# Kernel tuning notes

Hardware: AMD Instinct MI355X
Metric: run time of the kernel (lower is better)

## Reference

```python
import jax, jax.numpy as jnp
import numpy as np

B, S, D = 2, 2048, 2048
H = 16
Q_LORA, KV_LORA = 1536, 512
D_NOPE, D_ROPE = 128, 64
D_QK = D_NOPE + D_ROPE  # 192
D_V = 128
EPS = 1e-6
SCALE = D_QK ** -0.5


def rms_norm(x, w):
    var = jnp.mean(jnp.square(x), axis=-1, keepdims=True)
    return x * jax.lax.rsqrt(var + EPS) * w


def apply_rotary_emb(x, freqs_cis):
    # x: [B, S, h, dr]; freqs_cis: [S, dr//2, 2] (cos, sin); interleaved pairs
    b, s, h, dr = x.shape
    xp = x.reshape(b, s, h, dr // 2, 2)
    x0, x1 = xp[..., 0], xp[..., 1]
    cos = freqs_cis[None, :, None, :, 0]
    sin = freqs_cis[None, :, None, :, 1]
    o0 = x0 * cos - x1 * sin
    o1 = x0 * sin + x1 * cos
    return jnp.stack([o0, o1], axis=-1).reshape(b, s, h, dr)


def setup_inputs() -> dict:
    key = jax.random.key(0)
    ks = jax.random.split(key, 8)
    std = 0.02
    x = jax.random.normal(ks[0], (B, S, D), jnp.float32)
    inv_freq = 1.0 / (10000.0 ** (np.arange(0, D_ROPE, 2, dtype=np.float32) / D_ROPE))
    ang = np.outer(np.arange(S, dtype=np.float32), inv_freq)  # [S, 32]
    freqs_cis = jnp.asarray(np.stack([np.cos(ang), np.sin(ang)], axis=-1))
    return {
        'x': x,
        'freqs_cis': freqs_cis,
        'Wqa': jax.random.normal(ks[1], (Q_LORA, D), jnp.float32) * std,
        'q_a_ln_w': jnp.ones((Q_LORA,), jnp.float32),
        'Wqb': jax.random.normal(ks[2], (H * D_QK, Q_LORA), jnp.float32) * std,
        'Wkva': jax.random.normal(ks[3], (KV_LORA + D_ROPE, D), jnp.float32) * std,
        'kv_a_ln_w': jnp.ones((KV_LORA,), jnp.float32),
        'Wkvb': jax.random.normal(ks[4], (H * (D_NOPE + D_V), KV_LORA), jnp.float32) * std,
        'Wo': jax.random.normal(ks[5], (D, H * D_V), jnp.float32) * std,
    }


def reference(x, freqs_cis, Wqa, q_a_ln_w, Wqb, Wkva, kv_a_ln_w, Wkvb, Wo):
    # Low-rank Q projection: down -> RMSNorm -> up
    q = rms_norm(jnp.einsum('bsd,rd->bsr', x, Wqa), q_a_ln_w)
    q = jnp.einsum('bsr,er->bse', q, Wqb).reshape(B, S, H, D_QK)
    q_nope, q_pe = q[..., :D_NOPE], q[..., D_NOPE:]
    q = jnp.concatenate([q_nope, apply_rotary_emb(q_pe, freqs_cis)], axis=-1)

    # Low-rank KV projection with shared (MQA) rope part
    kv = jnp.einsum('bsd,ed->bse', x, Wkva)
    kv_c, k_pe = kv[..., :KV_LORA], kv[..., KV_LORA:]
    kv_c = rms_norm(kv_c, kv_a_ln_w)
    k_pe = apply_rotary_emb(k_pe[:, :, None, :], freqs_cis)  # [B,S,1,D_ROPE]
    kv = jnp.einsum('bsr,er->bse', kv_c, Wkvb).reshape(B, S, H, D_NOPE + D_V)
    k_nope, v = kv[..., :D_NOPE], kv[..., D_NOPE:]
    k = jnp.concatenate(
        [k_nope, jnp.broadcast_to(k_pe, (B, S, H, D_ROPE))], axis=-1)

    # Causal SDPA with scale = qk_head_dim ** -0.5
    scores = jnp.einsum('bqhd,bkhd->bhqk', q, k) * SCALE
    causal = jnp.tril(jnp.ones((S, S), bool))
    scores = jnp.where(causal[None, None], scores, jnp.finfo(scores.dtype).min)
    probs = jax.nn.softmax(scores, axis=-1)
    out = jnp.einsum('bhqk,bkhd->bqhd', probs, v).reshape(B, S, H * D_V)
    return jnp.einsum('bse,de->bsd', out, Wo)
```

## Files before the change

### kernel.cpp

```cpp
#include <hip/hip_runtime.h>
#include <math.h>

#define B_ 2
#define S_ 2048
#define D_ 2048
#define H_ 16
#define QLORA 1536
#define KVLORA 512
#define DN 128
#define DR 64
#define DQK 192
#define DV 128
#define EPSF 1e-6f
#define SCALEF 0.07216878364870322f

typedef short short8 __attribute__((ext_vector_type(8)));
typedef float float4v __attribute__((ext_vector_type(4)));

__device__ __forceinline__ unsigned short f2bf(float f) {
    union { float f; unsigned u; } x; x.f = f;
    unsigned r = x.u + 0x7fffu + ((x.u >> 16) & 1u);
    return (unsigned short)(r >> 16);
}
__device__ __forceinline__ float bf2f(unsigned short u) {
    union { unsigned u; float f; } x; x.u = (unsigned)u << 16;
    return x.f;
}

#define GLD16(src, dst)                                                        \
    __builtin_amdgcn_global_load_lds(                                          \
        (const __attribute__((address_space(1))) void*)(src),                  \
        (__attribute__((address_space(3))) void*)(dst), 16, 0, 0)

__global__ __launch_bounds__(256) void conv_all(
        const float* __restrict__ s0, unsigned short* __restrict__ d0, long e0,
        const float* __restrict__ s1, unsigned short* __restrict__ d1, long e1,
        const float* __restrict__ s2, unsigned short* __restrict__ d2, long e2,
        const float* __restrict__ s3, unsigned short* __restrict__ d3, long e3,
        const float* __restrict__ s4, unsigned short* __restrict__ d4, long e4,
        const float* __restrict__ s5, unsigned short* __restrict__ d5) {
    long c = (long)blockIdx.x * 256 + threadIdx.x;
    const float* src;
    unsigned short* dst;
    if      (c < e0) { src = s0; dst = d0; }
    else if (c < e1) { src = s1; dst = d1; c -= e0; }
    else if (c < e2) { src = s2; dst = d2; c -= e1; }
    else if (c < e3) { src = s3; dst = d3; c -= e2; }
    else if (c < e4) { src = s4; dst = d4; c -= e3; }
    else             { src = s5; dst = d5; c -= e4; }
    const float* p = src + c * 8;
    float4 a = *(const float4*)(p);
    float4 b = *(const float4*)(p + 4);
    union { short8 v; unsigned short u[8]; } t;
    t.u[0] = f2bf(a.x); t.u[1] = f2bf(a.y); t.u[2] = f2bf(a.z); t.u[3] = f2bf(a.w);
    t.u[4] = f2bf(b.x); t.u[5] = f2bf(b.y); t.u[6] = f2bf(b.z); t.u[7] = f2bf(b.w);
    *(short8*)&dst[c * 8] = t.v;
}

#define GBM 128
#define GBN 128
#define GBK 64

template <typename OT>
__global__ __launch_bounds__(256) void gemm_t(const unsigned short* __restrict__ A,
                                              const unsigned short* __restrict__ W,
                                              OT* __restrict__ C,
                                              int M, int N, int K) {
    __shared__ unsigned short As[GBM * GBK];
    __shared__ unsigned short Ws[GBN * GBK];

    const int tid = threadIdx.x;
    const int w = tid >> 6, lane = tid & 63;
    const int l16 = lane & 15, quad = lane >> 4;
    const int wm = (w >> 1) * 64, wn = (w & 1) * 64;
    const int row0 = blockIdx.y * GBM, col0 = blockIdx.x * GBN;

    const int rL  = lane >> 3;
    const int c8g = (lane & 7) ^ rL;
    const int swzk[2] = { (((0 * 4) + quad) ^ (l16 & 7)) * 8,
                          (((1 * 4) + quad) ^ (l16 & 7)) * 8 };

    const float4v zf = {0.f, 0.f, 0.f, 0.f};
    float4v acc[4][4] = {{zf, zf, zf, zf}, {zf, zf, zf, zf},
                         {zf, zf, zf, zf}, {zf, zf, zf, zf}};

    for (int k0 = 0; k0 < K; k0 += GBK) {
        __syncthreads();
#pragma unroll
        for (int j = 0; j < 4; ++j) {
            const int ch = w * 4 + j;
            const int r = ch * 8 + rL;
            GLD16(&A[(size_t)(row0 + r) * K + k0 + c8g * 8], &As[ch * 512]);
            GLD16(&W[(size_t)(col0 + r) * K + k0 + c8g * 8], &Ws[ch * 512]);
        }
        __syncthreads();

#pragma unroll
        for (int kk = 0; kk < 2; ++kk) {
            const int swz = swzk[kk];
            short8 af[4], bf[4];
#pragma unroll
            for (int mi = 0; mi < 4; ++mi)
                af[mi] = *(const short8*)&As[(wm + mi * 16 + l16) * GBK + swz];
#pragma unroll
            for (int ni = 0; ni < 4; ++ni)
                bf[ni] = *(const short8*)&Ws[(wn + ni * 16 + l16) * GBK + swz];
#pragma unroll
            for (int mi = 0; mi < 4; ++mi)
#pragma unroll
                for (int ni = 0; ni < 4; ++ni)
                    acc[mi][ni] = __builtin_amdgcn_mfma_f32_16x16x32_bf16(af[mi], bf[ni], acc[mi][ni], 0, 0, 0);
        }
    }

#pragma unroll
    for (int mi = 0; mi < 4; ++mi)
#pragma unroll
        for (int ni = 0; ni < 4; ++ni)
#pragma unroll
            for (int r = 0; r < 4; ++r) {
                size_t idx = (size_t)(row0 + wm + mi * 16 + quad * 4 + r) * N + col0 + wn + ni * 16 + l16;
                if constexpr (sizeof(OT) == 2) C[idx] = f2bf(acc[mi][ni][r]);
                else                           C[idx] = acc[mi][ni][r];
            }
}

__global__ __launch_bounds__(256) void rmsnorm_b(const float* __restrict__ X,
                                                 const float* __restrict__ w,
                                                 unsigned short* __restrict__ Y,
                                                 int n, int ld) {
    __shared__ float tmp[4];
    const int row = blockIdx.x;
    const int tid = threadIdx.x;
    const float* x = X + (size_t)row * ld;

    float ss = 0.f;
    for (int c = tid; c < n; c += 256) {
        float v = x[c];
        ss = fmaf(v, v, ss);
    }
#pragma unroll
    for (int off = 32; off; off >>= 1) ss += __shfl_xor(ss, off, 64);
    if ((tid & 63) == 0) tmp[tid >> 6] = ss;
    __syncthreads();
    ss = tmp[0] + tmp[1] + tmp[2] + tmp[3];
    float r = rsqrtf(ss / (float)n + EPSF);

    for (int c = tid; c < n; c += 256)
        Y[(size_t)row * n + c] = f2bf(x[c] * r * w[c]);
}

__global__ __launch_bounds__(256) void kv_post(const float* __restrict__ KV,
                                               const float* __restrict__ w,
                                               const float* __restrict__ fc,
                                               unsigned short* __restrict__ kvcb,
                                               float* __restrict__ kpe,
                                               int ldkv) {
    __shared__ float tmp[4];
    const int row = blockIdx.x;
    const int s = row & (S_ - 1);
    const int tid = threadIdx.x;
    const float* kv = KV + (size_t)row * ldkv;

    float ss = 0.f;
#pragma unroll
    for (int c = tid; c < KVLORA; c += 256) {
        float v = kv[c];
        ss = fmaf(v, v, ss);
    }
#pragma unroll
    for (int off = 32; off; off >>= 1) ss += __shfl_xor(ss, off, 64);
    if ((tid & 63) == 0) tmp[tid >> 6] = ss;
    __syncthreads();
    ss = tmp[0] + tmp[1] + tmp[2] + tmp[3];
    float r = rsqrtf(ss / (float)KVLORA + EPSF);

#pragma unroll
    for (int c = tid; c < KVLORA; c += 256)
        kvcb[(size_t)row * KVLORA + c] = f2bf(kv[c] * r * w[c]);

    if (tid < 32) {
        int i = tid;
        float c0 = fc[(s * 32 + i) * 2 + 0];
        float s0 = fc[(s * 32 + i) * 2 + 1];
        float x0 = kv[KVLORA + 2 * i];
        float x1 = kv[KVLORA + 2 * i + 1];
        kpe[(size_t)row * DR + 2 * i]     = x0 * c0 - x1 * s0;
        kpe[(size_t)row * DR + 2 * i + 1] = x0 * s0 + x1 * c0;
    }
}

__global__ __launch_bounds__(256) void pack_k(const unsigned short* __restrict__ kvbb,
                                              const float* __restrict__ kpe,
                                              unsigned short* __restrict__ Kbf) {
    const int c = blockIdx.x * 256 + threadIdx.x;
    const int total = B_ * H_ * S_ * (DQK / 8);
    if (c >= total) return;
    const int d8 = c % (DQK / 8);
    const int hs = c / (DQK / 8);
    const int s  = hs % S_;
    const int bh = hs / S_;
    const int b  = bh / H_;
    const int h  = bh % H_;
    const int d  = d8 * 8;
    const int row = b * S_ + s;

    short8 v;
    if (d < DN) {
        v = *(const short8*)&kvbb[(size_t)row * (H_ * 256) + h * 256 + d];
    } else {
        const float* src = kpe + (size_t)row * DR + (d - DN);
        float4 a = *(const float4*)(src);
        float4 bb = *(const float4*)(src + 4);
        union { short8 v; unsigned short u[8]; } t;
        t.u[0] = f2bf(a.x);  t.u[1] = f2bf(a.y);  t.u[2] = f2bf(a.z);  t.u[3] = f2bf(a.w);
        t.u[4] = f2bf(bb.x); t.u[5] = f2bf(bb.y); t.u[6] = f2bf(bb.z); t.u[7] = f2bf(bb.w);
        v = t.v;
    }
    *(short8*)&Kbf[(size_t)c * 8] = v;
}

__global__ __launch_bounds__(256) void pack_vt(const unsigned short* __restrict__ kvbb,
                                               unsigned short* __restrict__ Vt) {
    __shared__ unsigned short T[DV][72];
    const int st = blockIdx.x;
    const int bh = blockIdx.y;
    const int b = bh >> 4, h = bh & 15;
    const int s0 = st * 64;
    const int tid = threadIdx.x;

    for (int c = tid; c < 64 * 16; c += 256) {
        int sp = c >> 4, ch = c & 15;
        short8 v = *(const short8*)&kvbb[(size_t)(b * S_ + s0 + sp) * (H_ * 256) + h * 256 + DN + ch * 8];
        union { short8 v; unsigned short u[8]; } t; t.v = v;
        int dv = ch * 8;
#pragma unroll
        for (int e = 0; e < 8; ++e) T[dv + e][sp] = t.u[e];
    }
    __syncthreads();
    for (int c = tid; c < 128 * 8; c += 256) {
        int dv = c >> 3, ch = c & 7;
        *(short8*)&Vt[((size_t)bh * DV + dv) * S_ + s0 + ch * 8] = *(short8*)&T[dv][ch * 8];
    }
}

#define KROW 200
#define VROW 72
#define PROW 72
#define NQT 32

__global__ __launch_bounds__(256, 2) void flash_mfma(const unsigned short* __restrict__ Qb,
                                                     const float* __restrict__ fc,
                                                     const unsigned short* __restrict__ Kbf,
                                                     const unsigned short* __restrict__ Vt,
                                                     unsigned short* __restrict__ Ob) {
    __shared__ unsigned short Ks[64][KROW];
    __shared__ unsigned short Vs[DV][VROW];
    __shared__ unsigned short Ps[4][16][PROW];

    const int bh = blockIdx.x;
    const int bx = blockIdx.y;
    const int b = bh >> 4, h = bh & 15;
    const int tid = threadIdx.x;
    const int w = tid >> 6, lane = tid & 63;
    const int l16 = lane & 15, quad = lane >> 4;

    const unsigned short* Kg = Kbf + (size_t)bh * S_ * DQK;
    const unsigned short* Vg = Vt + (size_t)bh * DV * S_;

    for (int half = 0; half < 2; ++half) {
        const int qt = half ? (NQT - 1 - bx) : bx;
        const int q0 = qt * 64;
        const int ntiles = qt + 1;
        const int s = q0 + w * 16 + l16;

        short8 a_q[6];
        {
            const unsigned short* qrow = Qb + (size_t)(b * S_ + s) * (H_ * DQK) + h * DQK;
#pragma unroll
            for (int i = 0; i < 6; ++i) {
                short8 t = *(const short8*)&qrow[i * 32 + quad * 8];
                if (i >= 4) {
                    union { short8 v; unsigned short u[8]; } x; x.v = t;
#pragma unroll
                    for (int j = 0; j < 4; ++j) {
                        int ip = (i - 4) * 16 + quad * 4 + j;
                        float c0 = fc[(s * 32 + ip) * 2 + 0];
                        float s0 = fc[(s * 32 + ip) * 2 + 1];
                        float x0 = bf2f(x.u[2 * j]);
                        float x1 = bf2f(x.u[2 * j + 1]);
                        x.u[2 * j]     = f2bf(x0 * c0 - x1 * s0);
                        x.u[2 * j + 1] = f2bf(x0 * s0 + x1 * c0);
                    }
                    t = x.v;
                }
                a_q[i] = t;
            }
        }

        const float4v zf = {0.f, 0.f, 0.f, 0.f};
        float4v o_acc[8] = {zf, zf, zf, zf, zf, zf, zf, zf};
        float l_r[4] = {0.f, 0.f, 0.f, 0.f};

        short8 ldK[6], ldV[4];
#pragma unroll
        for (int i = 0; i < 6; ++i) {
            int c = tid + i * 256;
            int r = c / 24, cc = c % 24;
            ldK[i] = *(const short8*)&Kg[(size_t)r * DQK + cc * 8];
        }
#pragma unroll
        for (int i = 0; i < 4; ++i) {
            int c = tid + i * 256;
            int r = c >> 3, cc = c & 7;
            ldV[i] = *(const short8*)&Vg[(size_t)r * S_ + cc * 8];
        }

        for (int kt = 0; kt < ntiles; ++kt) {
            const int kbase = kt * 64;
            __syncthreads();
#pragma unroll
            for (int i = 0; i < 6; ++i) {
                int c = tid + i * 256;
                int r = c / 24, cc = c % 24;
                *(short8*)&Ks[r][cc * 8] = ldK[i];
            }
#pragma unroll
            for (int i = 0; i < 4; ++i) {
                int c = tid + i * 256;
                int r = c >> 3, cc = c & 7;
                *(short8*)&Vs[r][cc * 8] = ldV[i];
            }
            if (kt + 1 < ntiles) {
                const int kb2 = kbase + 64;
#pragma unroll
                for (int i = 0; i < 6; ++i) {
                    int c = tid + i * 256;
                    int r = c / 24, cc = c % 24;
                    ldK[i] = *(const short8*)&Kg[(size_t)(kb2 + r) * DQK + cc * 8];
                }
#pragma unroll
                for (int i = 0; i < 4; ++i) {
                    int c = tid + i * 256;
                    int r = c >> 3, cc = c & 7;
                    ldV[i] = *(const short8*)&Vg[(size_t)r * S_ + kb2 + cc * 8];
                }
            }
            __syncthreads();

            float4v sc[4] = {zf, zf, zf, zf};
#pragma unroll
            for (int kg = 0; kg < 4; ++kg) {
#pragma unroll
                for (int i = 0; i < 6; ++i) {
                    short8 bk = *(const short8*)&Ks[kg * 16 + l16][i * 32 + quad * 8];
                    sc[kg] = __builtin_amdgcn_mfma_f32_16x16x32_bf16(a_q[i], bk, sc[kg], 0, 0, 0);
                }
            }

            const bool last = (kt == ntiles - 1);
#pragma unroll
            for (int kg = 0; kg < 4; ++kg) {
                int key = kbase + kg * 16 + l16;
#pragma unroll
                for (int r = 0; r < 4; ++r) {
                    float sv = sc[kg][r] * SCALEF;
                    if (last && key > q0 + w * 16 + quad * 4 + r) sv = -1e30f;
                    float p = __expf(sv);
                    l_r[r] += p;
                    Ps[w][quad * 4 + r][kg * 16 + l16] = f2bf(p);
                }
            }

            __syncthreads();

#pragma unroll
            for (int kc = 0; kc < 2; ++kc) {
                short8 pa = *(const short8*)&Ps[w][l16][kc * 32 + quad * 8];
#pragma unroll
                for (int dvt = 0; dvt < 8; ++dvt) {
                    short8 vb = *(const short8*)&Vs[dvt * 16 + l16][kc * 32 + quad * 8];
                    o_acc[dvt] = __builtin_amdgcn_mfma_f32_16x16x32_bf16(pa, vb, o_acc[dvt], 0, 0, 0);
                }
            }
        }

#pragma unroll
        for (int r = 0; r < 4; ++r) {
            float t = l_r[r];
            t += __shfl_xor(t, 1);
            t += __shfl_xor(t, 2);
            t += __shfl_xor(t, 4);
            t += __shfl_xor(t, 8);
            l_r[r] = t;
        }
#pragma unroll
        for (int r = 0; r < 4; ++r) {
            float inv = 1.f / l_r[r];
            int row = q0 + w * 16 + quad * 4 + r;
            unsigned short* op = Ob + (size_t)(b * S_ + row) * (H_ * DV) + h * DV;
#pragma unroll
            for (int dvt = 0; dvt < 8; ++dvt)
                op[dvt * 16 + l16] = f2bf(o_acc[dvt][r] * inv);
        }
    }
}

extern "C" void kernel_launch(void* const* d_in, const int* in_sizes, int n_in,
                              void* d_out, int out_size, void* d_ws, size_t ws_size,
                              hipStream_t stream) {
    const float* x    = (const float*)d_in[0];
    const float* fc   = (const float*)d_in[1];
    const float* Wqa  = (const float*)d_in[2];
    const float* qlw  = (const float*)d_in[3];
    const float* Wqb  = (const float*)d_in[4];
    const float* Wkva = (const float*)d_in[5];
    const float* kvw  = (const float*)d_in[6];
    const float* Wkvb = (const float*)d_in[7];
    const float* Wo   = (const float*)d_in[8];
    float* out = (float*)d_out;

    const int M = B_ * S_;
    const int NQKV = QLORA + 640;
    char* wsb = (char*)d_ws;

    unsigned short* qb  = (unsigned short*)wsb;
    unsigned short* Wob = (unsigned short*)(wsb + 25165824);
    char* R2 = wsb + 50331648;
    float*          qlkv  = (float*)R2;
    unsigned short* xb    = (unsigned short*)(R2 + 35651584);
    unsigned short* Wcat  = (unsigned short*)(R2 + 52428800);
    unsigned short* kvbb  = (unsigned short*)R2;
    unsigned short* attnb = (unsigned short*)R2;
    char* R3 = R2 + 67108864;
    unsigned short* qlatb = (unsigned short*)R3;
    unsigned short* Wqbb  = (unsigned short*)(R3 + 12582912);
    unsigned short* Kbf   = (unsigned short*)R3;
    char* R4 = R3 + 25165824;
    float*          kpe   = (float*)R4;
    unsigned short* kvcb  = (unsigned short*)(R4 + 1048576);
    unsigned short* Wkvbb = (unsigned short*)(R4 + 5242880);
    unsigned short* Vt    = (unsigned short*)R4;

    {
        const long e0 = 1048576;
        const long e1 = e0 + 393216;
        const long e2 = e1 + 147456;
        const long e3 = e2 + 589824;
        const long e4 = e3 + 262144;
        const long tot = e4 + 524288;
        conv_all<<<(int)(tot / 256), 256, 0, stream>>>(
            x, xb, e0,
            Wqa, Wcat, e1,
            Wkva, Wcat + (size_t)QLORA * D_, e2,
            Wqb, Wqbb, e3,
            Wkvb, Wkvbb, e4,
            Wo, Wob);
    }

    gemm_t<float><<<dim3(NQKV / GBN, M / GBM), 256, 0, stream>>>(xb, Wcat, qlkv, M, NQKV, D_);

    rmsnorm_b<<<M, 256, 0, stream>>>(qlkv, qlw, qlatb, QLORA, NQKV);
    kv_post<<<M, 256, 0, stream>>>(qlkv + QLORA, kvw, fc, kvcb, kpe, NQKV);

    gemm_t<unsigned short><<<dim3(H_ * DQK / GBN, M / GBM), 256, 0, stream>>>(qlatb, Wqbb, qb, M, H_ * DQK, QLORA);
    gemm_t<unsigned short><<<dim3(H_ * 256 / GBN, M / GBM), 256, 0, stream>>>(kvcb, Wkvbb, kvbb, M, H_ * 256, KVLORA);

    {
        int total = B_ * H_ * S_ * (DQK / 8);
        pack_k<<<(total + 255) / 256, 256, 0, stream>>>(kvbb, kpe, Kbf);
        pack_vt<<<dim3(S_ / 64, B_ * H_), 256, 0, stream>>>(kvbb, Vt);
    }

    flash_mfma<<<dim3(B_ * H_, NQT / 2), 256, 0, stream>>>(qb, fc, Kbf, Vt, attnb);

    gemm_t<float><<<dim3(D_ / GBN, M / GBM), 256, 0, stream>>>(attnb, Wob, out, M, D_, D_);
}
```

Measured before the change: 449.8 us.

## Split long causal query tiles across KV halves and merge K/V pack kernels

Causal flash attention now launches one block per short query tile and two blocks per long query tile. Each of the two blocks covers half of the KV range and writes unnormalized fp32 partial outputs and row sums. A new combine kernel sums the two halves and normalizes them. Separately, the K pack and V transpose kernels are fused into one launch. The goal is finer, more even work per block and one fewer launch, at the cost of fp32 partial-output traffic, an extra combine kernel, and a reshuffled workspace layout.

Measured after the change: 488.7 us. 8.6% more time.

```diff
diff --git a/kernel.cpp b/kernel.cpp
--- a/kernel.cpp
+++ b/kernel.cpp
@@ -190,57 +190,58 @@
     }
 }
 
-__global__ __launch_bounds__(256) void pack_k(const unsigned short* __restrict__ kvbb,
-                                              const float* __restrict__ kpe,
-                                              unsigned short* __restrict__ Kbf) {
-    const int c = blockIdx.x * 256 + threadIdx.x;
-    const int total = B_ * H_ * S_ * (DQK / 8);
-    if (c >= total) return;
-    const int d8 = c % (DQK / 8);
-    const int hs = c / (DQK / 8);
-    const int s  = hs % S_;
-    const int bh = hs / S_;
-    const int b  = bh / H_;
-    const int h  = bh % H_;
-    const int d  = d8 * 8;
-    const int row = b * S_ + s;
-
-    short8 v;
-    if (d < DN) {
-        v = *(const short8*)&kvbb[(size_t)row * (H_ * 256) + h * 256 + d];
-    } else {
-        const float* src = kpe + (size_t)row * DR + (d - DN);
-        float4 a = *(const float4*)(src);
-        float4 bb = *(const float4*)(src + 4);
-        union { short8 v; unsigned short u[8]; } t;
-        t.u[0] = f2bf(a.x);  t.u[1] = f2bf(a.y);  t.u[2] = f2bf(a.z);  t.u[3] = f2bf(a.w);
-        t.u[4] = f2bf(bb.x); t.u[5] = f2bf(bb.y); t.u[6] = f2bf(bb.z); t.u[7] = f2bf(bb.w);
-        v = t.v;
-    }
-    *(short8*)&Kbf[(size_t)c * 8] = v;
-}
-
-__global__ __launch_bounds__(256) void pack_vt(const unsigned short* __restrict__ kvbb,
+#define NPK (B_ * H_ * S_ * (DQK / 8) / 256)
+
+__global__ __launch_bounds__(256) void pack_kv(const unsigned short* __restrict__ kvbb,
+                                               const float* __restrict__ kpe,
+                                               unsigned short* __restrict__ Kbf,
                                                unsigned short* __restrict__ Vt) {
     __shared__ unsigned short T[DV][72];
-    const int st = blockIdx.x;
-    const int bh = blockIdx.y;
-    const int b = bh >> 4, h = bh & 15;
-    const int s0 = st * 64;
     const int tid = threadIdx.x;
-
-    for (int c = tid; c < 64 * 16; c += 256) {
-        int sp = c >> 4, ch = c & 15;
-        short8 v = *(const short8*)&kvbb[(size_t)(b * S_ + s0 + sp) * (H_ * 256) + h * 256 + DN + ch * 8];
-        union { short8 v; unsigned short u[8]; } t; t.v = v;
-        int dv = ch * 8;
-#pragma unroll
-        for (int e = 0; e < 8; ++e) T[dv + e][sp] = t.u[e];
-    }
-    __syncthreads();
-    for (int c = tid; c < 128 * 8; c += 256) {
-        int dv = c >> 3, ch = c & 7;
-        *(short8*)&Vt[((size_t)bh * DV + dv) * S_ + s0 + ch * 8] = *(short8*)&T[dv][ch * 8];
+    if ((int)blockIdx.x < NPK) {
+        const int c = blockIdx.x * 256 + tid;
+        const int d8 = c % (DQK / 8);
+        const int hs = c / (DQK / 8);
+        const int s  = hs % S_;
+        const int bh = hs / S_;
+        const int b  = bh / H_;
+        const int h  = bh % H_;
+        const int d  = d8 * 8;
+        const int row = b * S_ + s;
+
+        short8 v;
+        if (d < DN) {
+            v = *(const short8*)&kvbb[(size_t)row * (H_ * 256) + h * 256 + d];
+        } else {
+            const float* src = kpe + (size_t)row * DR + (d - DN);
+            float4 a = *(const float4*)(src);
+            float4 bb = *(const float4*)(src + 4);
+            union { short8 v; unsigned short u[8]; } t;
+            t.u[0] = f2bf(a.x);  t.u[1] = f2bf(a.y);  t.u[2] = f2bf(a.z);  t.u[3] = f2bf(a.w);
+            t.u[4] = f2bf(bb.x); t.u[5] = f2bf(bb.y); t.u[6] = f2bf(bb.z); t.u[7] = f2bf(bb.w);
+            v = t.v;
+        }
+        *(short8*)&Kbf[(size_t)c * 8] = v;
+    } else {
+        const int id = blockIdx.x - NPK;
+        const int st = id & 31;
+        const int bh = id >> 5;
+        const int b = bh >> 4, h = bh & 15;
+        const int s0 = st * 64;
+
+        for (int c = tid; c < 64 * 16; c += 256) {
+            int sp = c >> 4, ch = c & 15;
+            short8 v = *(const short8*)&kvbb[(size_t)(b * S_ + s0 + sp) * (H_ * 256) + h * 256 + DN + ch * 8];
+            union { short8 v; unsigned short u[8]; } t; t.v = v;
+            int dv = ch * 8;
+#pragma unroll
+            for (int e = 0; e < 8; ++e) T[dv + e][sp] = t.u[e];
+        }
+        __syncthreads();
+        for (int c = tid; c < 128 * 8; c += 256) {
+            int dv = c >> 3, ch = c & 7;
+            *(short8*)&Vt[((size_t)bh * DV + dv) * S_ + s0 + ch * 8] = *(short8*)&T[dv][ch * 8];
+        }
     }
 }
 
@@ -249,151 +250,165 @@
 #define PROW 72
 #define NQT 32
 
-__global__ __launch_bounds__(256, 2) void flash_mfma(const unsigned short* __restrict__ Qb,
-                                                     const float* __restrict__ fc,
-                                                     const unsigned short* __restrict__ Kbf,
-                                                     const unsigned short* __restrict__ Vt,
-                                                     unsigned short* __restrict__ Ob) {
+__global__ __launch_bounds__(256, 2) void flash_split(const unsigned short* __restrict__ Qb,
+                                                      const float* __restrict__ fc,
+                                                      const unsigned short* __restrict__ Kbf,
+                                                      const unsigned short* __restrict__ Vt,
+                                                      unsigned short* __restrict__ Ob,
+                                                      float* __restrict__ Opart,
+                                                      float* __restrict__ Lpart) {
     __shared__ unsigned short Ks[64][KROW];
     __shared__ unsigned short Vs[DV][VROW];
     __shared__ unsigned short Ps[4][16][PROW];
 
     const int bh = blockIdx.x;
-    const int bx = blockIdx.y;
+    const int u  = blockIdx.y;
     const int b = bh >> 4, h = bh & 15;
     const int tid = threadIdx.x;
     const int w = tid >> 6, lane = tid & 63;
     const int l16 = lane & 15, quad = lane >> 4;
 
+    int qt, kt0, kt1, slot;
+    bool partial;
+    if (u < 16) { qt = u; kt0 = 0; kt1 = u + 1; partial = false; slot = 0; }
+    else {
+        int idx = u - 16;
+        qt = 16 + (idx >> 1);
+        slot = idx & 1;
+        int nt = qt + 1, mid = nt >> 1;
+        kt0 = slot ? mid : 0;
+        kt1 = slot ? nt : mid;
+        partial = true;
+    }
+    const int q0 = qt * 64;
+
     const unsigned short* Kg = Kbf + (size_t)bh * S_ * DQK;
     const unsigned short* Vg = Vt + (size_t)bh * DV * S_;
 
-    for (int half = 0; half < 2; ++half) {
-        const int qt = half ? (NQT - 1 - bx) : bx;
-        const int q0 = qt * 64;
-        const int ntiles = qt + 1;
-        const int s = q0 + w * 16 + l16;
-
-        short8 a_q[6];
-        {
-            const unsigned short* qrow = Qb + (size_t)(b * S_ + s) * (H_ * DQK) + h * DQK;
-#pragma unroll
-            for (int i = 0; i < 6; ++i) {
-                short8 t = *(const short8*)&qrow[i * 32 + quad * 8];
-                if (i >= 4) {
-                    union { short8 v; unsigned short u[8]; } x; x.v = t;
-#pragma unroll
-                    for (int j = 0; j < 4; ++j) {
-                        int ip = (i - 4) * 16 + quad * 4 + j;
-                        float c0 = fc[(s * 32 + ip) * 2 + 0];
-                        float s0 = fc[(s * 32 + ip) * 2 + 1];
-                        float x0 = bf2f(x.u[2 * j]);
-                        float x1 = bf2f(x.u[2 * j + 1]);
-                        x.u[2 * j]     = f2bf(x0 * c0 - x1 * s0);
-                        x.u[2 * j + 1] = f2bf(x0 * s0 + x1 * c0);
-                    }
-                    t = x.v;
+    const int s = q0 + w * 16 + l16;
+
+    short8 a_q[6];
+    {
+        const unsigned short* qrow = Qb + (size_t)(b * S_ + s) * (H_ * DQK) + h * DQK;
+#pragma unroll
+        for (int i = 0; i < 6; ++i) {
+            short8 t = *(const short8*)&qrow[i * 32 + quad * 8];
+            if (i >= 4) {
+                union { short8 v; unsigned short u[8]; } x; x.v = t;
+#pragma unroll
+                for (int j = 0; j < 4; ++j) {
+                    int ip = (i - 4) * 16 + quad * 4 + j;
+                    float c0 = fc[(s * 32 + ip) * 2 + 0];
+                    float s0 = fc[(s * 32 + ip) * 2 + 1];
+                    float x0 = bf2f(x.u[2 * j]);
+                    float x1 = bf2f(x.u[2 * j + 1]);
+                    x.u[2 * j]     = f2bf(x0 * c0 - x1 * s0);
+                    x.u[2 * j + 1] = f2bf(x0 * s0 + x1 * c0);
                 }
-                a_q[i] = t;
-            }
-        }
-
-        const float4v zf = {0.f, 0.f, 0.f, 0.f};
-        float4v o_acc[8] = {zf, zf, zf, zf, zf, zf, zf, zf};
-        float l_r[4] = {0.f, 0.f, 0.f, 0.f};
-
-        short8 ldK[6], ldV[4];
+                t = x.v;
+            }
+            a_q[i] = t;
+        }
+    }
+
+    const float4v zf = {0.f, 0.f, 0.f, 0.f};
+    float4v o_acc[8] = {zf, zf, zf, zf, zf, zf, zf, zf};
+    float l_r[4] = {0.f, 0.f, 0.f, 0.f};
+
+    short8 ldK[6], ldV[4];
+#pragma unroll
+    for (int i = 0; i < 6; ++i) {
+        int c = tid + i * 256;
+        int r = c / 24, cc = c % 24;
+        ldK[i] = *(const short8*)&Kg[(size_t)(kt0 * 64 + r) * DQK + cc * 8];
+    }
+#pragma unroll
+    for (int i = 0; i < 4; ++i) {
+        int c = tid + i * 256;
+        int r = c >> 3, cc = c & 7;
+        ldV[i] = *(const short8*)&Vg[(size_t)r * S_ + kt0 * 64 + cc * 8];
+    }
+
+    for (int kt = kt0; kt < kt1; ++kt) {
+        const int kbase = kt * 64;
+        __syncthreads();
 #pragma unroll
         for (int i = 0; i < 6; ++i) {
             int c = tid + i * 256;
             int r = c / 24, cc = c % 24;
-            ldK[i] = *(const short8*)&Kg[(size_t)r * DQK + cc * 8];
+            *(short8*)&Ks[r][cc * 8] = ldK[i];
         }
 #pragma unroll
         for (int i = 0; i < 4; ++i) {
             int c = tid + i * 256;
             int r = c >> 3, cc = c & 7;
-            ldV[i] = *(const short8*)&Vg[(size_t)r * S_ + cc * 8];
-        }
-
-        for (int kt = 0; kt < ntiles; ++kt) {
-            const int kbase = kt * 64;
-            __syncthreads();
+            *(short8*)&Vs[r][cc * 8] = ldV[i];
+        }
+        if (kt + 1 < kt1) {
+            const int kb2 = kbase + 64;
 #pragma unroll
             for (int i = 0; i < 6; ++i) {
                 int c = tid + i * 256;
                 int r = c / 24, cc = c % 24;
-                *(short8*)&Ks[r][cc * 8] = ldK[i];
+                ldK[i] = *(const short8*)&Kg[(size_t)(kb2 + r) * DQK + cc * 8];
             }
 #pragma unroll
             for (int i = 0; i < 4; ++i) {
                 int c = tid + i * 256;
                 int r = c >> 3, cc = c & 7;
-                *(short8*)&Vs[r][cc * 8] = ldV[i];
-            }
-            if (kt + 1 < ntiles) {
-                const int kb2 = kbase + 64;
-#pragma unroll
-                for (int i = 0; i < 6; ++i) {
-                    int c = tid + i * 256;
-                    int r = c / 24, cc = c % 24;
-                    ldK[i] = *(const short8*)&Kg[(size_t)(kb2 + r) * DQK + cc * 8];
-                }
-#pragma unroll
-                for (int i = 0; i < 4; ++i) {
-                    int c = tid + i * 256;
-                    int r = c >> 3, cc = c & 7;
-                    ldV[i] = *(const short8*)&Vg[(size_t)r * S_ + kb2 + cc * 8];
-                }
-            }
-            __syncthreads();
-
-            float4v sc[4] = {zf, zf, zf, zf};
-#pragma unroll
-            for (int kg = 0; kg < 4; ++kg) {
-#pragma unroll
-                for (int i = 0; i < 6; ++i) {
-                    short8 bk = *(const short8*)&Ks[kg * 16 + l16][i * 32 + quad * 8];
-                    sc[kg] = __builtin_amdgcn_mfma_f32_16x16x32_bf16(a_q[i], bk, sc[kg], 0, 0, 0);
-                }
-            }
-
-            const bool last = (kt == ntiles - 1);
-#pragma unroll
-            for (int kg = 0; kg < 4; ++kg) {
-                int key = kbase + kg * 16 + l16;
-#pragma unroll
-                for (int r = 0; r < 4; ++r) {
-                    float sv = sc[kg][r] * SCALEF;
-                    if (last && key > q0 + w * 16 + quad * 4 + r) sv = -1e30f;
-                    float p = __expf(sv);
-                    l_r[r] += p;
-                    Ps[w][quad * 4 + r][kg * 16 + l16] = f2bf(p);
-                }
-            }
-
-            __syncthreads();
-
-#pragma unroll
-            for (int kc = 0; kc < 2; ++kc) {
-                short8 pa = *(const short8*)&Ps[w][l16][kc * 32 + quad * 8];
-#pragma unroll
-                for (int dvt = 0; dvt < 8; ++dvt) {
-                    short8 vb = *(const short8*)&Vs[dvt * 16 + l16][kc * 32 + quad * 8];
-                    o_acc[dvt] = __builtin_amdgcn_mfma_f32_16x16x32_bf16(pa, vb, o_acc[dvt], 0, 0, 0);
-                }
-            }
-        }
-
-#pragma unroll
-        for (int r = 0; r < 4; ++r) {
-            float t = l_r[r];
-            t += __shfl_xor(t, 1);
-            t += __shfl_xor(t, 2);
-            t += __shfl_xor(t, 4);
-            t += __shfl_xor(t, 8);
-            l_r[r] = t;
-        }
+                ldV[i] = *(const short8*)&Vg[(size_t)r * S_ + kb2 + cc * 8];
+            }
+        }
+        __syncthreads();
+
+        float4v sc[4] = {zf, zf, zf, zf};
+#pragma unroll
+        for (int kg = 0; kg < 4; ++kg) {
+#pragma unroll
+            for (int i = 0; i < 6; ++i) {
+                short8 bk = *(const short8*)&Ks[kg * 16 + l16][i * 32 + quad * 8];
+                sc[kg] = __builtin_amdgcn_mfma_f32_16x16x32_bf16(a_q[i], bk, sc[kg], 0, 0, 0);
+            }
+        }
+
+        const bool diag = (kt == qt);
+#pragma unroll
+        for (int kg = 0; kg < 4; ++kg) {
+            int key = kbase + kg * 16 + l16;
+#pragma unroll
+            for (int r = 0; r < 4; ++r) {
+                float sv = sc[kg][r] * SCALEF;
+                if (diag && key > q0 + w * 16 + quad * 4 + r) sv = -1e30f;
+                float p = __expf(sv);
+                l_r[r] += p;
+                Ps[w][quad * 4 + r][kg * 16 + l16] = f2bf(p);
+            }
+        }
+
+        __syncthreads();
+
+#pragma unroll
+        for (int kc = 0; kc < 2; ++kc) {
+            short8 pa = *(const short8*)&Ps[w][l16][kc * 32 + quad * 8];
+#pragma unroll
+            for (int dvt = 0; dvt < 8; ++dvt) {
+                short8 vb = *(const short8*)&Vs[dvt * 16 + l16][kc * 32 + quad * 8];
+                o_acc[dvt] = __builtin_amdgcn_mfma_f32_16x16x32_bf16(pa, vb, o_acc[dvt], 0, 0, 0);
+            }
+        }
+    }
+
+#pragma unroll
+    for (int r = 0; r < 4; ++r) {
+        float t = l_r[r];
+        t += __shfl_xor(t, 1);
+        t += __shfl_xor(t, 2);
+        t += __shfl_xor(t, 4);
+        t += __shfl_xor(t, 8);
+        l_r[r] = t;
+    }
+
+    if (!partial) {
 #pragma unroll
         for (int r = 0; r < 4; ++r) {
             float inv = 1.f / l_r[r];
@@ -403,6 +418,39 @@
             for (int dvt = 0; dvt < 8; ++dvt)
                 op[dvt * 16 + l16] = f2bf(o_acc[dvt][r] * inv);
         }
+    } else {
+        const size_t sb = ((size_t)(bh * 16 + (qt - 16)) * 2 + slot);
+        float* ob = Opart + sb * 8192;
+#pragma unroll
+        for (int r = 0; r < 4; ++r) {
+            int row = w * 16 + quad * 4 + r;
+#pragma unroll
+            for (int dvt = 0; dvt < 8; ++dvt)
+                ob[(size_t)row * DV + dvt * 16 + l16] = o_acc[dvt][r];
+            if (l16 == 0) Lpart[sb * 64 + row] = l_r[r];
+        }
+    }
+}
+
+__global__ __launch_bounds__(256) void norm_comb(const float* __restrict__ Opart,
+                                                 const float* __restrict__ Lpart,
+                                                 unsigned short* __restrict__ Ob) {
+    __shared__ float ls[64];
+    const int t = blockIdx.x;
+    const int bh = t >> 4, j = t & 15;
+    const int qt = 16 + j;
+    const int b = bh >> 4, h = bh & 15;
+    const int tid = threadIdx.x;
+    const size_t ob0 = (size_t)t * 2 * 8192, ob1 = ob0 + 8192;
+    const size_t lb0 = (size_t)t * 2 * 64, lb1 = lb0 + 64;
+
+    if (tid < 64) ls[tid] = Lpart[lb0 + tid] + Lpart[lb1 + tid];
+    __syncthreads();
+
+    for (int idx = tid; idx < 64 * DV; idx += 256) {
+        int row = idx >> 7, col = idx & 127;
+        float o = Opart[ob0 + idx] + Opart[ob1 + idx];
+        Ob[(size_t)(b * S_ + qt * 64 + row) * (H_ * DV) + h * DV + col] = f2bf(o / ls[row]);
     }
 }
 
@@ -426,20 +474,22 @@
 
     unsigned short* qb  = (unsigned short*)wsb;
     unsigned short* Wob = (unsigned short*)(wsb + 25165824);
+    float*          kpe = (float*)(wsb + 33554432);
     char* R2 = wsb + 50331648;
     float*          qlkv  = (float*)R2;
     unsigned short* xb    = (unsigned short*)(R2 + 35651584);
     unsigned short* Wcat  = (unsigned short*)(R2 + 52428800);
     unsigned short* kvbb  = (unsigned short*)R2;
     unsigned short* attnb = (unsigned short*)R2;
+    float*          Opart = (float*)(R2 + 16777216);
+    float*          Lpart = (float*)(R2 + 50331648);
     char* R3 = R2 + 67108864;
     unsigned short* qlatb = (unsigned short*)R3;
     unsigned short* Wqbb  = (unsigned short*)(R3 + 12582912);
     unsigned short* Kbf   = (unsigned short*)R3;
     char* R4 = R3 + 25165824;
-    float*          kpe   = (float*)R4;
-    unsigned short* kvcb  = (unsigned short*)(R4 + 1048576);
-    unsigned short* Wkvbb = (unsigned short*)(R4 + 5242880);
+    unsigned short* kvcb  = (unsigned short*)R4;
+    unsigned short* Wkvbb = (unsigned short*)(R4 + 4194304);
     unsigned short* Vt    = (unsigned short*)R4;
 
     {
@@ -466,13 +516,11 @@
     gemm_t<unsigned short><<<dim3(H_ * DQK / GBN, M / GBM), 256, 0, stream>>>(qlatb, Wqbb, qb, M, H_ * DQK, QLORA);
     gemm_t<unsigned short><<<dim3(H_ * 256 / GBN, M / GBM), 256, 0, stream>>>(kvcb, Wkvbb, kvbb, M, H_ * 256, KVLORA);
 
-    {
-        int total = B_ * H_ * S_ * (DQK / 8);
-        pack_k<<<(total + 255) / 256, 256, 0, stream>>>(kvbb, kpe, Kbf);
-        pack_vt<<<dim3(S_ / 64, B_ * H_), 256, 0, stream>>>(kvbb, Vt);
-    }
-
-    flash_mfma<<<dim3(B_ * H_, NQT / 2), 256, 0, stream>>>(qb, fc, Kbf, Vt, attnb);
+    pack_kv<<<NPK + 1024, 256, 0, stream>>>(kvbb, kpe, Kbf, Vt);
+
+    flash_split<<<dim3(B_ * H_, 48), 256, 0, stream>>>(qb, fc, Kbf, Vt, attnb, Opart, Lpart);
+
+    norm_comb<<<B_ * H_ * 16, 256, 0, stream>>>(Opart, Lpart, attnb);
 
     gemm_t<float><<<dim3(D_ / GBN, M / GBM), 256, 0, stream>>>(attnb, Wob, out, M, D_, D_);
 }
```

## Process paired causal query tiles concurrently with 512-thread flash blocks; fuse K/V packing

Applied to the files above, without the earlier changes.

The flash attention kernel now runs both paired query tiles (short and long causal extents) at the same time in one 512-thread block. Each half of the warps owns one tile and they share the K/V tile loads, instead of walking the two tiles one after the other. Warps of the short tile sit idle once their tiles are done, but the K/V shared-memory traffic is amortised and there is more parallelism per block. The separate pack_k and pack_vt kernels are merged into one launch, and kpe is moved in the workspace so its buffer does not overlap Vt.

Measured after the change: 459.2 us. 2.1% more time.

```diff
diff --git a/kernel.cpp b/kernel.cpp
--- a/kernel.cpp
+++ b/kernel.cpp
@@ -190,57 +190,58 @@
     }
 }
 
-__global__ __launch_bounds__(256) void pack_k(const unsigned short* __restrict__ kvbb,
-                                              const float* __restrict__ kpe,
-                                              unsigned short* __restrict__ Kbf) {
-    const int c = blockIdx.x * 256 + threadIdx.x;
-    const int total = B_ * H_ * S_ * (DQK / 8);
-    if (c >= total) return;
-    const int d8 = c % (DQK / 8);
-    const int hs = c / (DQK / 8);
-    const int s  = hs % S_;
-    const int bh = hs / S_;
-    const int b  = bh / H_;
-    const int h  = bh % H_;
-    const int d  = d8 * 8;
-    const int row = b * S_ + s;
-
-    short8 v;
-    if (d < DN) {
-        v = *(const short8*)&kvbb[(size_t)row * (H_ * 256) + h * 256 + d];
-    } else {
-        const float* src = kpe + (size_t)row * DR + (d - DN);
-        float4 a = *(const float4*)(src);
-        float4 bb = *(const float4*)(src + 4);
-        union { short8 v; unsigned short u[8]; } t;
-        t.u[0] = f2bf(a.x);  t.u[1] = f2bf(a.y);  t.u[2] = f2bf(a.z);  t.u[3] = f2bf(a.w);
-        t.u[4] = f2bf(bb.x); t.u[5] = f2bf(bb.y); t.u[6] = f2bf(bb.z); t.u[7] = f2bf(bb.w);
-        v = t.v;
-    }
-    *(short8*)&Kbf[(size_t)c * 8] = v;
-}
-
-__global__ __launch_bounds__(256) void pack_vt(const unsigned short* __restrict__ kvbb,
+#define NPK (B_ * H_ * S_ * (DQK / 8) / 256)
+
+__global__ __launch_bounds__(256) void pack_kv(const unsigned short* __restrict__ kvbb,
+                                               const float* __restrict__ kpe,
+                                               unsigned short* __restrict__ Kbf,
                                                unsigned short* __restrict__ Vt) {
     __shared__ unsigned short T[DV][72];
-    const int st = blockIdx.x;
-    const int bh = blockIdx.y;
-    const int b = bh >> 4, h = bh & 15;
-    const int s0 = st * 64;
     const int tid = threadIdx.x;
-
-    for (int c = tid; c < 64 * 16; c += 256) {
-        int sp = c >> 4, ch = c & 15;
-        short8 v = *(const short8*)&kvbb[(size_t)(b * S_ + s0 + sp) * (H_ * 256) + h * 256 + DN + ch * 8];
-        union { short8 v; unsigned short u[8]; } t; t.v = v;
-        int dv = ch * 8;
-#pragma unroll
-        for (int e = 0; e < 8; ++e) T[dv + e][sp] = t.u[e];
-    }
-    __syncthreads();
-    for (int c = tid; c < 128 * 8; c += 256) {
-        int dv = c >> 3, ch = c & 7;
-        *(short8*)&Vt[((size_t)bh * DV + dv) * S_ + s0 + ch * 8] = *(short8*)&T[dv][ch * 8];
+    if ((int)blockIdx.x < NPK) {
+        const int c = blockIdx.x * 256 + tid;
+        const int d8 = c % (DQK / 8);
+        const int hs = c / (DQK / 8);
+        const int s  = hs % S_;
+        const int bh = hs / S_;
+        const int b  = bh / H_;
+        const int h  = bh % H_;
+        const int d  = d8 * 8;
+        const int row = b * S_ + s;
+
+        short8 v;
+        if (d < DN) {
+            v = *(const short8*)&kvbb[(size_t)row * (H_ * 256) + h * 256 + d];
+        } else {
+            const float* src = kpe + (size_t)row * DR + (d - DN);
+            float4 a = *(const float4*)(src);
+            float4 bb = *(const float4*)(src + 4);
+            union { short8 v; unsigned short u[8]; } t;
+            t.u[0] = f2bf(a.x);  t.u[1] = f2bf(a.y);  t.u[2] = f2bf(a.z);  t.u[3] = f2bf(a.w);
+            t.u[4] = f2bf(bb.x); t.u[5] = f2bf(bb.y); t.u[6] = f2bf(bb.z); t.u[7] = f2bf(bb.w);
+            v = t.v;
+        }
+        *(short8*)&Kbf[(size_t)c * 8] = v;
+    } else {
+        const int id = blockIdx.x - NPK;
+        const int st = id & 31;
+        const int bh = id >> 5;
+        const int b = bh >> 4, h = bh & 15;
+        const int s0 = st * 64;
+
+        for (int c = tid; c < 64 * 16; c += 256) {
+            int sp = c >> 4, ch = c & 15;
+            short8 v = *(const short8*)&kvbb[(size_t)(b * S_ + s0 + sp) * (H_ * 256) + h * 256 + DN + ch * 8];
+            union { short8 v; unsigned short u[8]; } t; t.v = v;
+            int dv = ch * 8;
+#pragma unroll
+            for (int e = 0; e < 8; ++e) T[dv + e][sp] = t.u[e];
+        }
+        __syncthreads();
+        for (int c = tid; c < 128 * 8; c += 256) {
+            int dv = c >> 3, ch = c & 7;
+            *(short8*)&Vt[((size_t)bh * DV + dv) * S_ + s0 + ch * 8] = *(short8*)&T[dv][ch * 8];
+        }
     }
 }
 
@@ -249,14 +250,14 @@
 #define PROW 72
 #define NQT 32
 
-__global__ __launch_bounds__(256, 2) void flash_mfma(const unsigned short* __restrict__ Qb,
+__global__ __launch_bounds__(512, 4) void flash_mfma(const unsigned short* __restrict__ Qb,
                                                      const float* __restrict__ fc,
                                                      const unsigned short* __restrict__ Kbf,
                                                      const unsigned short* __restrict__ Vt,
                                                      unsigned short* __restrict__ Ob) {
     __shared__ unsigned short Ks[64][KROW];
     __shared__ unsigned short Vs[DV][VROW];
-    __shared__ unsigned short Ps[4][16][PROW];
+    __shared__ unsigned short Ps[8][16][PROW];
 
     const int bh = blockIdx.x;
     const int bx = blockIdx.y;
@@ -264,90 +265,94 @@
     const int tid = threadIdx.x;
     const int w = tid >> 6, lane = tid & 63;
     const int l16 = lane & 15, quad = lane >> 4;
+    const int ws = w & 3;
+
+    const int qt = (w >= 4) ? bx : (NQT - 1 - bx);
+    const int q0 = qt * 64;
+    const int myNt = qt + 1;
+    const int ntA = NQT - bx;
 
     const unsigned short* Kg = Kbf + (size_t)bh * S_ * DQK;
     const unsigned short* Vg = Vt + (size_t)bh * DV * S_;
 
-    for (int half = 0; half < 2; ++half) {
-        const int qt = half ? (NQT - 1 - bx) : bx;
-        const int q0 = qt * 64;
-        const int ntiles = qt + 1;
-        const int s = q0 + w * 16 + l16;
-
-        short8 a_q[6];
-        {
-            const unsigned short* qrow = Qb + (size_t)(b * S_ + s) * (H_ * DQK) + h * DQK;
-#pragma unroll
-            for (int i = 0; i < 6; ++i) {
-                short8 t = *(const short8*)&qrow[i * 32 + quad * 8];
-                if (i >= 4) {
-                    union { short8 v; unsigned short u[8]; } x; x.v = t;
-#pragma unroll
-                    for (int j = 0; j < 4; ++j) {
-                        int ip = (i - 4) * 16 + quad * 4 + j;
-                        float c0 = fc[(s * 32 + ip) * 2 + 0];
-                        float s0 = fc[(s * 32 + ip) * 2 + 1];
-                        float x0 = bf2f(x.u[2 * j]);
-                        float x1 = bf2f(x.u[2 * j + 1]);
-                        x.u[2 * j]     = f2bf(x0 * c0 - x1 * s0);
-                        x.u[2 * j + 1] = f2bf(x0 * s0 + x1 * c0);
-                    }
-                    t = x.v;
+    const int s = q0 + ws * 16 + l16;
+
+    short8 a_q[6];
+    {
+        const unsigned short* qrow = Qb + (size_t)(b * S_ + s) * (H_ * DQK) + h * DQK;
+#pragma unroll
+        for (int i = 0; i < 6; ++i) {
+            short8 t = *(const short8*)&qrow[i * 32 + quad * 8];
+            if (i >= 4) {
+                union { short8 v; unsigned short u[8]; } x; x.v = t;
+#pragma unroll
+                for (int j = 0; j < 4; ++j) {
+                    int ip = (i - 4) * 16 + quad * 4 + j;
+                    float c0 = fc[(s * 32 + ip) * 2 + 0];
+                    float s0 = fc[(s * 32 + ip) * 2 + 1];
+                    float x0 = bf2f(x.u[2 * j]);
+                    float x1 = bf2f(x.u[2 * j + 1]);
+                    x.u[2 * j]     = f2bf(x0 * c0 - x1 * s0);
+                    x.u[2 * j + 1] = f2bf(x0 * s0 + x1 * c0);
                 }
-                a_q[i] = t;
-            }
-        }
-
-        const float4v zf = {0.f, 0.f, 0.f, 0.f};
-        float4v o_acc[8] = {zf, zf, zf, zf, zf, zf, zf, zf};
-        float l_r[4] = {0.f, 0.f, 0.f, 0.f};
-
-        short8 ldK[6], ldV[4];
-#pragma unroll
-        for (int i = 0; i < 6; ++i) {
-            int c = tid + i * 256;
+                t = x.v;
+            }
+            a_q[i] = t;
+        }
+    }
+
+    const float4v zf = {0.f, 0.f, 0.f, 0.f};
+    float4v o_acc[8] = {zf, zf, zf, zf, zf, zf, zf, zf};
+    float l_r[4] = {0.f, 0.f, 0.f, 0.f};
+
+    short8 ldK[3], ldV[2];
+#pragma unroll
+    for (int i = 0; i < 3; ++i) {
+        int c = tid + i * 512;
+        int r = c / 24, cc = c % 24;
+        ldK[i] = *(const short8*)&Kg[(size_t)r * DQK + cc * 8];
+    }
+#pragma unroll
+    for (int i = 0; i < 2; ++i) {
+        int c = tid + i * 512;
+        int r = c >> 3, cc = c & 7;
+        ldV[i] = *(const short8*)&Vg[(size_t)r * S_ + cc * 8];
+    }
+
+    for (int kt = 0; kt < ntA; ++kt) {
+        const int kbase = kt * 64;
+        const bool active = (kt < myNt);
+        __syncthreads();
+#pragma unroll
+        for (int i = 0; i < 3; ++i) {
+            int c = tid + i * 512;
             int r = c / 24, cc = c % 24;
-            ldK[i] = *(const short8*)&Kg[(size_t)r * DQK + cc * 8];
-        }
-#pragma unroll
-        for (int i = 0; i < 4; ++i) {
-            int c = tid + i * 256;
+            *(short8*)&Ks[r][cc * 8] = ldK[i];
+        }
+#pragma unroll
+        for (int i = 0; i < 2; ++i) {
+            int c = tid + i * 512;
             int r = c >> 3, cc = c & 7;
-            ldV[i] = *(const short8*)&Vg[(size_t)r * S_ + cc * 8];
-        }
-
-        for (int kt = 0; kt < ntiles; ++kt) {
-            const int kbase = kt * 64;
-            __syncthreads();
-#pragma unroll
-            for (int i = 0; i < 6; ++i) {
-                int c = tid + i * 256;
+            *(short8*)&Vs[r][cc * 8] = ldV[i];
+        }
+        if (kt + 1 < ntA) {
+            const int kb2 = kbase + 64;
+#pragma unroll
+            for (int i = 0; i < 3; ++i) {
+                int c = tid + i * 512;
                 int r = c / 24, cc = c % 24;
-                *(short8*)&Ks[r][cc * 8] = ldK[i];
-            }
-#pragma unroll
-            for (int i = 0; i < 4; ++i) {
-                int c = tid + i * 256;
+                ldK[i] = *(const short8*)&Kg[(size_t)(kb2 + r) * DQK + cc * 8];
+            }
+#pragma unroll
+            for (int i = 0; i < 2; ++i) {
+                int c = tid + i * 512;
                 int r = c >> 3, cc = c & 7;
-                *(short8*)&Vs[r][cc * 8] = ldV[i];
-            }
-            if (kt + 1 < ntiles) {
-                const int kb2 = kbase + 64;
-#pragma unroll
-                for (int i = 0; i < 6; ++i) {
-                    int c = tid + i * 256;
-                    int r = c / 24, cc = c % 24;
-                    ldK[i] = *(const short8*)&Kg[(size_t)(kb2 + r) * DQK + cc * 8];
-                }
-#pragma unroll
-                for (int i = 0; i < 4; ++i) {
-                    int c = tid + i * 256;
-                    int r = c >> 3, cc = c & 7;
-                    ldV[i] = *(const short8*)&Vg[(size_t)r * S_ + kb2 + cc * 8];
-                }
-            }
-            __syncthreads();
-
+                ldV[i] = *(const short8*)&Vg[(size_t)r * S_ + kb2 + cc * 8];
+            }
+        }
+        __syncthreads();
+
+        if (active) {
             float4v sc[4] = {zf, zf, zf, zf};
 #pragma unroll
             for (int kg = 0; kg < 4; ++kg) {
@@ -358,22 +363,24 @@
                 }
             }
 
-            const bool last = (kt == ntiles - 1);
+            const bool diag = (kt == qt);
 #pragma unroll
             for (int kg = 0; kg < 4; ++kg) {
                 int key = kbase + kg * 16 + l16;
 #pragma unroll
                 for (int r = 0; r < 4; ++r) {
                     float sv = sc[kg][r] * SCALEF;
-                    if (last && key > q0 + w * 16 + quad * 4 + r) sv = -1e30f;
+                    if (diag && key > q0 + ws * 16 + quad * 4 + r) sv = -1e30f;
                     float p = __expf(sv);
                     l_r[r] += p;
                     Ps[w][quad * 4 + r][kg * 16 + l16] = f2bf(p);
                 }
             }
-
-            __syncthreads();
-
+        }
+
+        __syncthreads();
+
+        if (active) {
 #pragma unroll
             for (int kc = 0; kc < 2; ++kc) {
                 short8 pa = *(const short8*)&Ps[w][l16][kc * 32 + quad * 8];
@@ -384,25 +391,25 @@
                 }
             }
         }
-
-#pragma unroll
-        for (int r = 0; r < 4; ++r) {
-            float t = l_r[r];
-            t += __shfl_xor(t, 1);
-            t += __shfl_xor(t, 2);
-            t += __shfl_xor(t, 4);
-            t += __shfl_xor(t, 8);
-            l_r[r] = t;
-        }
-#pragma unroll
-        for (int r = 0; r < 4; ++r) {
-            float inv = 1.f / l_r[r];
-            int row = q0 + w * 16 + quad * 4 + r;
-            unsigned short* op = Ob + (size_t)(b * S_ + row) * (H_ * DV) + h * DV;
-#pragma unroll
-            for (int dvt = 0; dvt < 8; ++dvt)
-                op[dvt * 16 + l16] = f2bf(o_acc[dvt][r] * inv);
-        }
+    }
+
+#pragma unroll
+    for (int r = 0; r < 4; ++r) {
+        float t = l_r[r];
+        t += __shfl_xor(t, 1);
+        t += __shfl_xor(t, 2);
+        t += __shfl_xor(t, 4);
+        t += __shfl_xor(t, 8);
+        l_r[r] = t;
+    }
+#pragma unroll
+    for (int r = 0; r < 4; ++r) {
+        float inv = 1.f / l_r[r];
+        int row = q0 + ws * 16 + quad * 4 + r;
+        unsigned short* op = Ob + (size_t)(b * S_ + row) * (H_ * DV) + h * DV;
+#pragma unroll
+        for (int dvt = 0; dvt < 8; ++dvt)
+            op[dvt * 16 + l16] = f2bf(o_acc[dvt][r] * inv);
     }
 }
 
@@ -426,6 +433,7 @@
 
     unsigned short* qb  = (unsigned short*)wsb;
     unsigned short* Wob = (unsigned short*)(wsb + 25165824);
+    float*          kpe = (float*)(wsb + 33554432);
     char* R2 = wsb + 50331648;
     float*          qlkv  = (float*)R2;
     unsigned short* xb    = (unsigned short*)(R2 + 35651584);
@@ -437,9 +445,8 @@
     unsigned short* Wqbb  = (unsigned short*)(R3 + 12582912);
     unsigned short* Kbf   = (unsigned short*)R3;
     char* R4 = R3 + 25165824;
-    float*          kpe   = (float*)R4;
-    unsigned short* kvcb  = (unsigned short*)(R4 + 1048576);
-    unsigned short* Wkvbb = (unsigned short*)(R4 + 5242880);
+    unsigned short* kvcb  = (unsigned short*)R4;
+    unsigned short* Wkvbb = (unsigned short*)(R4 + 4194304);
     unsigned short* Vt    = (unsigned short*)R4;
 
     {
@@ -466,13 +473,9 @@
     gemm_t<unsigned short><<<dim3(H_ * DQK / GBN, M / GBM), 256, 0, stream>>>(qlatb, Wqbb, qb, M, H_ * DQK, QLORA);
     gemm_t<unsigned short><<<dim3(H_ * 256 / GBN, M / GBM), 256, 0, stream>>>(kvcb, Wkvbb, kvbb, M, H_ * 256, KVLORA);
 
-    {
-        int total = B_ * H_ * S_ * (DQK / 8);
-        pack_k<<<(total + 255) / 256, 256, 0, stream>>>(kvbb, kpe, Kbf);
-        pack_vt<<<dim3(S_ / 64, B_ * H_), 256, 0, stream>>>(kvbb, Vt);
-    }
-
-    flash_mfma<<<dim3(B_ * H_, NQT / 2), 256, 0, stream>>>(qb, fc, Kbf, Vt, attnb);
+    pack_kv<<<NPK + 1024, 256, 0, stream>>>(kvbb, kpe, Kbf, Vt);
+
+    flash_mfma<<<dim3(B_ * H_, NQT / 2), 512, 0, stream>>>(qb, fc, Kbf, Vt, attnb);
 
     gemm_t<float><<<dim3(D_ / GBN, M / GBM), 256, 0, stream>>>(attnb, Wob, out, M, D_, D_);
 }
```
